# Performance work log

Hardware: AMD Instinct MI355X
Metric: run time of the kernel (lower is better)

The kernel has to match this reference:

```python
import jax, jax.numpy as jnp
import numpy as np

WS = 8
NUM_HEADS = 4
DIM = 64
H = W = 128
B = 16
EPS = 1e-5


def _rel_pos_index(ws):
    coords = np.stack(np.meshgrid(np.arange(ws), np.arange(ws), indexing='ij'))  # (2,ws,ws)
    cf = coords.reshape(2, -1)
    rel = (cf[:, :, None] - cf[:, None, :]).transpose(1, 2, 0).astype(np.int64)
    rel[..., 0] += ws - 1
    rel[..., 1] += ws - 1
    rel[..., 0] *= 2 * ws - 1
    return jnp.asarray(rel.sum(-1))  # (ws*ws, ws*ws)

_RPI = _rel_pos_index(WS)


def _ln_hw(x, g, b):
    # LayerNorm over last two dims (H,W) of (B,C,H,W), affine shape (H,W)
    mu = x.mean(axis=(-2, -1), keepdims=True)
    var = ((x - mu) ** 2).mean(axis=(-2, -1), keepdims=True)
    return (x - mu) / jnp.sqrt(var + EPS) * g + b


def _ln_c(x, g, b):
    mu = x.mean(-1, keepdims=True)
    var = ((x - mu) ** 2).mean(-1, keepdims=True)
    return (x - mu) / jnp.sqrt(var + EPS) * g + b


def _win_part(x, ws):
    # (B,C,H,W) -> (B*nW, ws*ws, C)
    b, c, hh, ww = x.shape
    x = x.reshape(b, c, hh // ws, ws, ww // ws, ws)
    return x.transpose(0, 2, 4, 3, 5, 1).reshape(b * (hh // ws) * (ww // ws), ws * ws, c)


def _win_rev(w, ws, hh, ww, b):
    # (B*nW, ws*ws, C) -> (B,C,H,W)
    c = w.shape[-1]
    w = w.reshape(b, hh // ws, ww // ws, ws, ws, c)
    return w.transpose(0, 5, 1, 3, 2, 4).reshape(b, c, hh, ww)


def _forward(x, lclg1_ln1_g, lclg1_ln1_b, lclg1_conv_w, lclg1_conv_b, lclg1_ln2_g, lclg1_ln2_b,
             lclg2_ln1_g, lclg2_ln1_b, lclg2_conv_w, lclg2_conv_b, lclg2_ln2_g, lclg2_ln2_b,
             pos1, pos2, q_w, q_b, kv_w, kv_b, rpb_table, gamma, proj_w, proj_b,
             norm2_g, norm2_b, fc1_w, fc1_b, fc2_w, fc2_b):
    b, c, hh, ww = x.shape
    h = NUM_HEADS
    hd = c // h
    n = WS * WS
    scale = hd ** -0.5

    def lclg(z, g1, b1, cw, cb, g2, b2):
        z = _ln_hw(z, g1, b1)
        z = jnp.einsum('oc,bchw->bohw', cw, z) + cb[None, :, None, None]  # 1x1 conv
        return jax.nn.gelu(_ln_hw(z, g2, b2), approximate=False)

    x1 = lclg(x, lclg1_ln1_g, lclg1_ln1_b, lclg1_conv_w, lclg1_conv_b, lclg1_ln2_g, lclg1_ln2_b)
    x2 = lclg(x, lclg2_ln1_g, lclg2_ln1_b, lclg2_conv_w, lclg2_conv_b, lclg2_ln2_g, lclg2_ln2_b)

    x1w = _win_part(x1, WS) + pos1  # (B_, N, C)
    x2w = _win_part(x2, WS) + pos2
    bw = x1w.shape[0]

    q = (x1w @ q_w.T + q_b).reshape(bw, n, h, hd).transpose(0, 2, 1, 3) * scale  # (B_,h,N,hd)
    kv = (x2w @ kv_w.T + kv_b).reshape(bw, n, 2, h, hd).transpose(2, 0, 3, 1, 4)
    k, v = kv[0], kv[1]

    attn = jnp.einsum('bhnd,bhmd->bhnm', q, k)
    bias = rpb_table[_RPI.reshape(-1)].reshape(n, n, h).transpose(2, 0, 1)  # (h,N,N)
    attn = jax.nn.softmax(attn + bias[None], axis=-1)
    o = jnp.einsum('bhnm,bhmd->bhnd', attn, v)  # (B_,h,N,hd)

    # LAM_Module: attention over head_dim channels of (B_,h,N,hd)
    y = o.transpose(0, 3, 1, 2).reshape(bw, hd, h * n)  # (B_,hd,h*N)
    energy = jnp.einsum('bik,bjk->bij', y, y)  # (B_,hd,hd)
    lam = jnp.einsum('bij,bjk->bik', jax.nn.softmax(energy, axis=-1), y)
    y = (gamma * lam + y).reshape(bw, hd, h, n).transpose(0, 2, 3, 1)  # (B_,h,N,hd)

    xo = y.transpose(0, 2, 1, 3).reshape(bw, n, c) + q.transpose(0, 2, 1, 3).reshape(bw, n, c) + x1w
    xo = xo @ proj_w.T + proj_b

    xo = _win_rev(xo, WS, hh, ww, b)  # (B,C,H,W)

    # MLP with pre-norm residual over channel dim
    t = xo.reshape(b, c, hh * ww).transpose(0, 2, 1)  # (B,HW,C)
    tn = _ln_c(t, norm2_g, norm2_b)
    t = t + (jax.nn.gelu(tn @ fc1_w.T + fc1_b, approximate=False) @ fc2_w.T + fc2_b)
    return t.transpose(0, 2, 1).reshape(b, c, hh, ww)


def setup_inputs() -> dict:
    key = jax.random.key(0)
    ks = jax.random.split(key, 16)
    d = DIM

    def rn(i, shape, sc=0.02):
        return jax.random.normal(ks[i], shape, jnp.float32) * sc

    return dict(
        x=jax.random.normal(ks[0], (B, d, H, W), jnp.float32),
        lclg1_ln1_g=jnp.ones((H, W), jnp.float32), lclg1_ln1_b=jnp.zeros((H, W), jnp.float32),
        lclg1_conv_w=rn(1, (d, d)), lclg1_conv_b=jnp.zeros((d,), jnp.float32),
        lclg1_ln2_g=jnp.ones((H, W), jnp.float32), lclg1_ln2_b=jnp.zeros((H, W), jnp.float32),
        lclg2_ln1_g=jnp.ones((H, W), jnp.float32), lclg2_ln1_b=jnp.zeros((H, W), jnp.float32),
        lclg2_conv_w=rn(2, (d, d)), lclg2_conv_b=jnp.zeros((d,), jnp.float32),
        lclg2_ln2_g=jnp.ones((H, W), jnp.float32), lclg2_ln2_b=jnp.zeros((H, W), jnp.float32),
        pos1=jnp.ones((1, WS * WS, d), jnp.float32),
        pos2=jnp.ones((1, WS * WS, d), jnp.float32),
        q_w=rn(3, (d, d)), q_b=jnp.zeros((d,), jnp.float32),
        kv_w=rn(4, (2 * d, d)), kv_b=jnp.zeros((2 * d,), jnp.float32),
        rpb_table=rn(5, ((2 * WS - 1) ** 2, NUM_HEADS)),
        gamma=jnp.full((1,), 0.1, jnp.float32),
        proj_w=rn(6, (d, d)), proj_b=jnp.zeros((d,), jnp.float32),
        norm2_g=jnp.ones((d,), jnp.float32), norm2_b=jnp.zeros((d,), jnp.float32),
        fc1_w=rn(7, (d, d)), fc1_b=jnp.zeros((d,), jnp.float32),
        fc2_w=rn(8, (d, d)), fc2_b=jnp.zeros((d,), jnp.float32),
    )


def reference(x, lclg1_ln1_g, lclg1_ln1_b, lclg1_conv_w, lclg1_conv_b, lclg1_ln2_g, lclg1_ln2_b,
              lclg2_ln1_g, lclg2_ln1_b, lclg2_conv_w, lclg2_conv_b, lclg2_ln2_g, lclg2_ln2_b,
              pos1, pos2, q_w, q_b, kv_w, kv_b, rpb_table, gamma, proj_w, proj_b,
              norm2_g, norm2_b, fc1_w, fc1_b, fc2_w, fc2_b):
    return _forward(x, lclg1_ln1_g, lclg1_ln1_b, lclg1_conv_w, lclg1_conv_b, lclg1_ln2_g, lclg1_ln2_b,
                    lclg2_ln1_g, lclg2_ln1_b, lclg2_conv_w, lclg2_conv_b, lclg2_ln2_g, lclg2_ln2_b,
                    pos1, pos2, q_w, q_b, kv_w, kv_b, rpb_table, gamma, proj_w, proj_b,
                    norm2_g, norm2_b, fc1_w, fc1_b, fc2_w, fc2_b)
```

## Files before the change

### kernel.cpp

```cpp
#include <hip/hip_runtime.h>
#include <hip/hip_bf16.h>

typedef __hip_bfloat16 bf16;
typedef __attribute__((ext_vector_type(8))) short short8;
typedef __attribute__((ext_vector_type(4))) short short4v;
typedef __attribute__((ext_vector_type(4))) float float4v;
typedef __attribute__((ext_vector_type(2))) float float2v;

__device__ __forceinline__ short f2bs(float f){
    union { bf16 h; short s; } u; u.h = __float2bfloat16(f); return u.s;
}
__device__ __forceinline__ float bs2f(short s){
    return __uint_as_float(((unsigned)(unsigned short)s) << 16);
}
__device__ __forceinline__ float gelu_exact(float x){
    float ax = fabsf(x) * 0.70710678118654752440f;
    float t  = __builtin_amdgcn_rcpf(fmaf(0.3275911f, ax, 1.0f));
    float poly = t*fmaf(t, fmaf(t, fmaf(t, fmaf(t, 1.061405429f, -1.453152027f),
                                 1.421413741f), -0.284496736f), 0.254829592f);
    float e = __expf(-ax*ax);
    float erfp = fmaf(-poly, e, 1.0f);
    float er = copysignf(erfp, x);
    return 0.5f * x * (1.0f + er);
}
#define MFMA(a,b,c) __builtin_amdgcn_mfma_f32_16x16x32_bf16((a),(b),(c),0,0,0)

#define HW 16384
#define NPLANE 1048576
#define EPS 1e-5f
#define LS 72

#define OFF_W1   0
#define OFF_W2   4096
#define OFF_QW   8192
#define OFF_KVW  12288
#define OFF_PW   20480
#define OFF_FW1  24576
#define OFF_FW2  28672

__global__ __launch_bounds__(256) void k_pre(const float* __restrict__ x,
                                             float* __restrict__ mu,
                                             float* __restrict__ rinv,
                                             const float* __restrict__ w1, const float* __restrict__ w2,
                                             const float* __restrict__ qw, const float* __restrict__ kvw,
                                             const float* __restrict__ pw, const float* __restrict__ fw1,
                                             const float* __restrict__ fw2,
                                             short* __restrict__ wb, float* __restrict__ rowsum){
    int bi = blockIdx.x;
    int tid = threadIdx.x;
    if (bi < 1024){
        const float* p = x + (size_t)bi * HW;
        float s = 0.f, ss = 0.f;
        for (int i = tid; i < HW/4; i += 256){
            float4v v = *(const float4v*)(p + i*4);
            #pragma unroll
            for (int k = 0; k < 4; k++){ s += v[k]; ss += v[k]*v[k]; }
        }
        __shared__ float rs[256], rss[256];
        rs[tid] = s; rss[tid] = ss; __syncthreads();
        for (int st = 128; st > 0; st >>= 1){
            if (tid < st){ rs[tid] += rs[tid+st]; rss[tid] += rss[tid+st]; }
            __syncthreads();
        }
        if (tid == 0){
            float m = rs[0] * (1.f/HW);
            float v = rss[0] * (1.f/HW) - m*m;
            mu[bi] = m; rinv[bi] = rsqrtf(v + EPS);
        }
    } else if (bi < 1032){
        int wi = bi - 1024;
        const float* src = wi==0?w1: wi==1?w2: wi==2?qw: wi==3?kvw: wi==4?(kvw+4096): wi==5?pw: wi==6?fw1: fw2;
        short* dst = wb + wi*4096;
        int base = tid*16;
        short8 o8[2];
        #pragma unroll
        for (int k = 0; k < 2; k++){
            float4v v0 = *(const float4v*)(src + base + 8*k);
            float4v v1 = *(const float4v*)(src + base + 8*k + 4);
            #pragma unroll
            for (int j = 0; j < 4; j++){ o8[k][j] = f2bs(v0[j]); o8[k][4+j] = f2bs(v1[j]); }
        }
        *(short8*)&dst[base]     = o8[0];
        *(short8*)&dst[base + 8] = o8[1];
    } else {
        if (tid < 128){
            int br = tid >> 6, o = tid & 63;
            const float* W = br ? w2 : w1;
            float s = 0.f;
            for (int c = 0; c < 64; c++) s += W[o*64 + c];
            rowsum[br*64 + o] = s;
        }
    }
}

__global__ __launch_bounds__(256, 4) void k_conv(const float* __restrict__ x,
                                              const float* __restrict__ mu,
                                              const float* __restrict__ rinv,
                                              const float* __restrict__ g1a, const float* __restrict__ b1a,
                                              const float* __restrict__ cb1,
                                              const float* __restrict__ g1b, const float* __restrict__ b1b,
                                              const float* __restrict__ cb2,
                                              const short* __restrict__ wb,
                                              const float* __restrict__ rowsum,
                                              float* __restrict__ partS, float* __restrict__ partQ){
    int blk = blockIdx.x;
    int b = blk >> 6; int chunk = blk & 63;
    __shared__ __align__(16) short xn_bf[64*LS];
    const int tid = threadIdx.x;
    const int wq = tid >> 6, lane = tid & 63, qd = lane >> 4, col = lane & 15;
    const float4v zf = {0.f,0.f,0.f,0.f};
    const int p = tid & 63, cq = tid >> 6;

    float4v m4[4], r4[4];
    #pragma unroll
    for (int k = 0; k < 4; k++){
        m4[k] = *(const float4v*)(mu   + b*64 + 16*cq + 4*k);
        r4[k] = *(const float4v*)(rinv + b*64 + 16*cq + 4*k);
    }
    short8 a10 = *(const short8*)&wb[OFF_W1 + (16*wq + col)*64 + 8*qd];
    short8 a11 = *(const short8*)&wb[OFF_W1 + (16*wq + col)*64 + 32 + 8*qd];
    short8 a20 = *(const short8*)&wb[OFF_W2 + (16*wq + col)*64 + 8*qd];
    short8 a21 = *(const short8*)&wb[OFF_W2 + (16*wq + col)*64 + 32 + 8*qd];
    float cb1v[4], rs1v[4], cb2v[4], rs2v[4];
    #pragma unroll
    for (int r = 0; r < 4; r++){
        int o = 16*wq + 4*qd + r;
        cb1v[r] = cb1[o]; rs1v[r] = rowsum[o];
        cb2v[r] = cb2[o]; rs2v[r] = rowsum[64 + o];
    }
    float sa[2][4]  = {{0.f,0.f,0.f,0.f},{0.f,0.f,0.f,0.f}};
    float ssa[2][4] = {{0.f,0.f,0.f,0.f},{0.f,0.f,0.f,0.f}};

    for (int tl = 0; tl < 4; tl++){
        int hw0 = chunk*256 + tl*64;
        {
            const float* xb = x + (size_t)(b*64 + 16*cq)*HW + hw0 + p;
            short8 o8[2];
            #pragma unroll
            for (int k = 0; k < 2; k++)
                #pragma unroll
                for (int j = 0; j < 8; j++){
                    int jj = 8*k + j;
                    float v = xb[(size_t)jj*HW];
                    o8[k][j] = f2bs((v - m4[jj>>2][jj&3]) * r4[jj>>2][jj&3]);
                }
            *(short8*)&xn_bf[p*LS + 16*cq]     = o8[0];
            *(short8*)&xn_bf[p*LS + 16*cq + 8] = o8[1];
        }
        __syncthreads();
        #pragma unroll
        for (int jn = 0; jn < 4; jn++){
            short8 bx0 = *(const short8*)&xn_bf[(16*jn + col)*LS + 8*qd];
            short8 bx1 = *(const short8*)&xn_bf[(16*jn + col)*LS + 32 + 8*qd];
            int hw = hw0 + 16*jn + col;
            {
                float4v acc = zf;
                acc = MFMA(a10, bx0, acc);
                acc = MFMA(a11, bx1, acc);
                float gl = g1a[hw], bl = b1a[hw];
                #pragma unroll
                for (int r = 0; r < 4; r++){
                    float v = gl*acc[r] + bl*rs1v[r] + cb1v[r];
                    sa[0][r] += v; ssa[0][r] += v*v;
                }
            }
            {
                float4v acc = zf;
                acc = MFMA(a20, bx0, acc);
                acc = MFMA(a21, bx1, acc);
                float gl = g1b[hw], bl = b1b[hw];
                #pragma unroll
                for (int r = 0; r < 4; r++){
                    float v = gl*acc[r] + bl*rs2v[r] + cb2v[r];
                    sa[1][r] += v; ssa[1][r] += v*v;
                }
            }
        }
        __syncthreads();
    }

    #pragma unroll
    for (int br = 0; br < 2; br++)
        #pragma unroll
        for (int r = 0; r < 4; r++){
            float s = sa[br][r], ss = ssa[br][r];
            s += __shfl_xor(s, 1); ss += __shfl_xor(ss, 1);
            s += __shfl_xor(s, 2); ss += __shfl_xor(ss, 2);
            s += __shfl_xor(s, 4); ss += __shfl_xor(ss, 4);
            s += __shfl_xor(s, 8); ss += __shfl_xor(ss, 8);
            if (col == 0){
                int o = 16*wq + 4*qd + r;
                size_t pi = ((size_t)(br*16 + b)*64 + o)*64 + chunk;
                partS[pi] = s; partQ[pi] = ss;
            }
        }
}

__global__ __launch_bounds__(256) void k_fin(const float* __restrict__ partS,
                                             const float* __restrict__ partQ,
                                             float* __restrict__ mu2,
                                             float* __restrict__ rinv2){
    int row = blockIdx.x*4 + (threadIdx.x >> 6);
    int lane = threadIdx.x & 63;
    float s  = partS[(size_t)row*64 + lane];
    float ss = partQ[(size_t)row*64 + lane];
    #pragma unroll
    for (int st = 1; st < 64; st <<= 1){
        s  += __shfl_xor(s,  st);
        ss += __shfl_xor(ss, st);
    }
    if (lane == 0){
        float m = s * (1.f/HW);
        float v = ss * (1.f/HW) - m*m;
        mu2[row] = m; rinv2[row] = rsqrtf(v + EPS);
    }
}

__global__ __launch_bounds__(256, 4) void k_attn(const float* __restrict__ x, float* __restrict__ outp,
                                              const float* __restrict__ mu1, const float* __restrict__ rinv1,
                                              const float* __restrict__ rowsum,
                                              const float* __restrict__ cb1, const float* __restrict__ cb2,
                                              const float* __restrict__ g1a, const float* __restrict__ b1a,
                                              const float* __restrict__ g1b, const float* __restrict__ b1b,
                                              const float* __restrict__ mu2, const float* __restrict__ rinv2,
                                              const float* __restrict__ g2a, const float* __restrict__ b2a,
                                              const float* __restrict__ g2b, const float* __restrict__ b2b,
                                              const float* __restrict__ pos1, const float* __restrict__ pos2,
                                              const short* __restrict__ wb,
                                              const float* __restrict__ qb, const float* __restrict__ kvb,
                                              const float* __restrict__ rpb, const float* __restrict__ gammap,
                                              const float* __restrict__ pb,
                                              const float* __restrict__ n2g, const float* __restrict__ n2b,
                                              const float* __restrict__ fb1,
                                              const float* __restrict__ fb2){
    int B = blockIdx.x;
    int hy = (B & 7) | ((B >> 5) & 8);
    int wx = (((B >> 9) & 7) << 1) | ((B >> 3) & 1);
    int b  = (B >> 4) & 15;

    const short* qwb  = wb + OFF_QW;
    const short* kvwb = wb + OFF_KVW;
    const short* pwb  = wb + OFF_PW;
    const short* f1b  = wb + OFF_FW1;
    const short* f2b  = wb + OFF_FW2;

    __shared__ __align__(16) char smem[40464];
    short* bufA = (short*)smem;
    short* bufK = (short*)(smem + 9216);
    short* bufV = (short*)(smem + 18432);
    short* bufQ = (short*)(smem + 27648);
    float* rpb_lds = (float*)(smem + 36864);
    float* energyS = (float*)(smem + 36864);
    short* soft_bf = (short*)(smem + 37888);
    float* XOf  = (float*)(smem + 18432);
    short* tnb  = (short*)smem;
    short* h1b  = (short*)(smem + 9216);
    float* sumS = (float*)(smem + 36864);
    float* sqS  = (float*)(smem + 37888);
    float* muS  = (float*)(smem + 38912);
    float* rinvS= (float*)(smem + 39168);

    const int tid = threadIdx.x;
    const int wq = tid >> 6, lane = tid & 63, qd = lane >> 4, col = lane & 15;
    size_t base = (size_t)b * NPLANE;
    #define HWOF(t) ((hy*8 + ((t)>>3))*128 + wx*8 + ((t)&7))

    const float4v zf = {0.f,0.f,0.f,0.f};
    const short8 zero8 = {0,0,0,0,0,0,0,0};

    for (int i = tid; i < 900; i += 256) rpb_lds[i] = rpb[i];

    {
        int t = tid & 63, cq = tid >> 6;
        int hw = HWOF(t);
        const float* mup = mu1   + b*64 + 16*cq;
        const float* rvp = rinv1 + b*64 + 16*cq;
        float4v m4[4], r4[4];
        #pragma unroll
        for (int k = 0; k < 4; k++){
            m4[k] = *(const float4v*)(mup + 4*k);
            r4[k] = *(const float4v*)(rvp + 4*k);
        }
        short8 o8[2];
        #pragma unroll
        for (int k = 0; k < 2; k++)
            #pragma unroll
            for (int j = 0; j < 8; j++){
                int jj = 8*k + j;
                float v = x[base + (size_t)(16*cq + jj)*HW + hw];
                o8[k][j] = f2bs((v - m4[jj>>2][jj&3]) * r4[jj>>2][jj&3]);
            }
        *(short8*)&bufV[t*LS + 16*cq]     = o8[0];
        *(short8*)&bufV[t*LS + 16*cq + 8] = o8[1];
    }
    __syncthreads();

    {
        short8 a10 = *(const short8*)&wb[OFF_W1 + (16*wq + col)*64 + 8*qd];
        short8 a11 = *(const short8*)&wb[OFF_W1 + (16*wq + col)*64 + 32 + 8*qd];
        short8 a20 = *(const short8*)&wb[OFF_W2 + (16*wq + col)*64 + 8*qd];
        short8 a21 = *(const short8*)&wb[OFF_W2 + (16*wq + col)*64 + 32 + 8*qd];
        float cb1v[4], rs1v[4], m2a[4], rv2a[4];
        float cb2v[4], rs2v[4], m2b[4], rv2b[4];
        #pragma unroll
        for (int r = 0; r < 4; r++){
            int o = 16*wq + 4*qd + r;
            cb1v[r] = cb1[o]; rs1v[r] = rowsum[o];
            m2a[r] = mu2[b*64 + o]; rv2a[r] = rinv2[b*64 + o];
            cb2v[r] = cb2[o]; rs2v[r] = rowsum[64 + o];
            m2b[r] = mu2[1024 + b*64 + o]; rv2b[r] = rinv2[1024 + b*64 + o];
        }
        #pragma unroll
        for (int jn = 0; jn < 4; jn++){
            int t = 16*jn + col; int hw = HWOF(t);
            short8 bx0 = *(const short8*)&bufV[t*LS + 8*qd];
            short8 bx1 = *(const short8*)&bufV[t*LS + 32 + 8*qd];
            {
                float4v acc = zf;
                acc = MFMA(a10, bx0, acc);
                acc = MFMA(a11, bx1, acc);
                float gl = g1a[hw], bl = b1a[hw], gg = g2a[hw], bo = b2a[hw];
                float4v p4 = *(const float4v*)(pos1 + t*64 + 16*wq + 4*qd);
                short4v pk;
                #pragma unroll
                for (int r = 0; r < 4; r++){
                    float v = gl*acc[r] + bl*rs1v[r] + cb1v[r];
                    float z = (v - m2a[r]) * rv2a[r] * gg + bo;
                    pk[r] = f2bs(gelu_exact(z) + p4[r]);
                }
                *(short4v*)&bufA[t*LS + 16*wq + 4*qd] = pk;
            }
            {
                float4v acc = zf;
                acc = MFMA(a20, bx0, acc);
                acc = MFMA(a21, bx1, acc);
                float gl = g1b[hw], bl = b1b[hw], gg = g2b[hw], bo = b2b[hw];
                float4v p4 = *(const float4v*)(pos2 + t*64 + 16*wq + 4*qd);
                short4v pk;
                #pragma unroll
                for (int r = 0; r < 4; r++){
                    float v = gl*acc[r] + bl*rs2v[r] + cb2v[r];
                    float z = (v - m2b[r]) * rv2b[r] * gg + bo;
                    pk[r] = f2bs(gelu_exact(z) + p4[r]);
                }
                *(short4v*)&bufQ[t*LS + 16*wq + 4*qd] = pk;
            }
        }
    }
    __syncthreads();

    {
        short8 ax0 = *(const short8*)&bufQ[(16*wq + col)*LS + 8*qd];
        short8 ax1 = *(const short8*)&bufQ[(16*wq + col)*LS + 32 + 8*qd];
        #pragma unroll
        for (int jn = 0; jn < 4; jn++){
            int c = 16*jn + col;
            short8 wv0 = *(const short8*)&kvwb[(64 + c)*64 + 8*qd];
            short8 wv1 = *(const short8*)&kvwb[(64 + c)*64 + 32 + 8*qd];
            float4v acc = zf;
            acc = MFMA(ax0, wv0, acc);
            acc = MFMA(ax1, wv1, acc);
            float bv = kvb[64 + c];
            short4v pk;
            #pragma unroll
            for (int r = 0; r < 4; r++) pk[r] = f2bs(acc[r] + bv);
            *(short4v*)&bufV[c*LS + 16*wq + 4*qd] = pk;
        }
        short8 a0 = *(const short8*)&kvwb[(16*wq + col)*64 + 8*qd];
        short8 a1 = *(const short8*)&kvwb[(16*wq + col)*64 + 32 + 8*qd];
        float kbr[4];
        #pragma unroll
        for (int r = 0; r < 4; r++) kbr[r] = kvb[16*wq + 4*qd + r];
        #pragma unroll
        for (int jn = 0; jn < 4; jn++){
            int t = 16*jn + col;
            short8 bx0 = *(const short8*)&bufQ[t*LS + 8*qd];
            short8 bx1 = *(const short8*)&bufQ[t*LS + 32 + 8*qd];
            float4v acc = zf;
            acc = MFMA(a0, bx0, acc);
            acc = MFMA(a1, bx1, acc);
            short4v pk;
            #pragma unroll
            for (int r = 0; r < 4; r++) pk[r] = f2bs(acc[r] + kbr[r]);
            *(short4v*)&bufK[t*LS + 16*wq + 4*qd] = pk;
        }
    }
    __syncthreads();

    {
        short8 a0 = *(const short8*)&qwb[(16*wq + col)*64 + 8*qd];
        short8 a1 = *(const short8*)&qwb[(16*wq + col)*64 + 32 + 8*qd];
        float qbr[4];
        #pragma unroll
        for (int r = 0; r < 4; r++) qbr[r] = qb[16*wq + 4*qd + r];
        #pragma unroll
        for (int jn = 0; jn < 4; jn++){
            int t = 16*jn + col;
            short8 bx0 = *(const short8*)&bufA[t*LS + 8*qd];
            short8 bx1 = *(const short8*)&bufA[t*LS + 32 + 8*qd];
            float4v acc = zf;
            acc = MFMA(a0, bx0, acc);
            acc = MFMA(a1, bx1, acc);
            short4v pk;
            #pragma unroll
            for (int r = 0; r < 4; r++) pk[r] = f2bs((acc[r] + qbr[r]) * 0.25f);
            *(short4v*)&bufQ[t*LS + 16*wq + 4*qd] = pk;
        }
    }
    short4v xreg[4];
    #pragma unroll
    for (int h = 0; h < 4; h++){
        short4v xr;
        #pragma unroll
        for (int r = 0; r < 4; r++)
            xr[r] = bufA[(16*wq + 4*qd + r)*LS + 16*h + col];
        xreg[h] = xr;
    }
    __syncthreads();

    int idx_t[4][4];
    {
        int t = 16*wq + col, ty = t >> 3, tx = t & 7;
        #pragma unroll
        for (int jn = 0; jn < 4; jn++)
            #pragma unroll
            for (int r = 0; r < 4; r++){
                int u = 16*jn + 4*qd + r;
                idx_t[jn][r] = (ty - (u>>3) + 7)*15 + (tx - (u&7) + 7);
            }
    }

    for (int h = 0; h < 4; h++){
        short8 bq = *(const short8*)&bufQ[(16*wq + col)*LS + h*16 + (qd & 1)*8];
        float pr[4][4];
        #pragma unroll
        for (int jn = 0; jn < 4; jn++){
            short8 ak = *(const short8*)&bufK[(16*jn + col)*LS + h*16 + (qd & 1)*8];
            if (qd >= 2) ak = zero8;
            float4v acc = MFMA(ak, bq, zf);
            #pragma unroll
            for (int r = 0; r < 4; r++)
                pr[jn][r] = acc[r] + rpb_lds[idx_t[jn][r]*4 + h];
        }
        float m = pr[0][0];
        #pragma unroll
        for (int jn = 0; jn < 4; jn++)
            #pragma unroll
            for (int r = 0; r < 4; r++) m = fmaxf(m, pr[jn][r]);
        m = fmaxf(m, __shfl_xor(m, 16));
        m = fmaxf(m, __shfl_xor(m, 32));
        float s = 0.f;
        #pragma unroll
        for (int jn = 0; jn < 4; jn++)
            #pragma unroll
            for (int r = 0; r < 4; r++){ pr[jn][r] = __expf(pr[jn][r] - m); s += pr[jn][r]; }
        s += __shfl_xor(s, 16);
        s += __shfl_xor(s, 32);
        float rc = 1.f / s;
        #pragma unroll
        for (int jn = 0; jn < 4; jn++){
            short4v pk;
            #pragma unroll
            for (int r = 0; r < 4; r++) pk[r] = f2bs(pr[jn][r] * rc);
            *(short4v*)&bufA[(16*wq + col)*LS + 16*jn + 4*qd] = pk;
        }
        short8 ap0 = *(const short8*)&bufA[(16*wq + col)*LS + 8*qd];
        short8 ap1 = *(const short8*)&bufA[(16*wq + col)*LS + 32 + 8*qd];
        short8 bv0 = *(const short8*)&bufV[(h*16 + col)*LS + 8*qd];
        short8 bv1 = *(const short8*)&bufV[(h*16 + col)*LS + 32 + 8*qd];
        float4v acc_o = zf;
        acc_o = MFMA(ap0, bv0, acc_o);
        acc_o = MFMA(ap1, bv1, acc_o);
        __syncthreads();
        short4v ot;
        #pragma unroll
        for (int r = 0; r < 4; r++) ot[r] = f2bs(acc_o[r]);
        *(short4v*)&bufV[(h*16 + col)*LS + 16*wq + 4*qd] = ot;
        #pragma unroll
        for (int r = 0; r < 4; r++)
            bufK[(16*wq + 4*qd + r)*LS + h*16 + col] = ot[r];
    }
    __syncthreads();

    {
        float4v acc_e = zf;
        #pragma unroll
        for (int h = 0; h < 4; h++){
            short8 f0 = *(const short8*)&bufV[(h*16 + col)*LS + 8*qd];
            short8 f1 = *(const short8*)&bufV[(h*16 + col)*LS + 32 + 8*qd];
            acc_e = MFMA(f0, f0, acc_e);
            acc_e = MFMA(f1, f1, acc_e);
        }
        if (wq == 0){
            #pragma unroll
            for (int r = 0; r < 4; r++) energyS[(4*qd + r)*16 + col] = acc_e[r];
        }
    }
    __syncthreads();
    if (tid < 16){
        int i = tid; float m = -1e30f;
        for (int j = 0; j < 16; j++) m = fmaxf(m, energyS[i*16 + j]);
        float s = 0.f; float e[16];
        for (int j = 0; j < 16; j++){ e[j] = __expf(energyS[i*16 + j] - m); s += e[j]; }
        float rc = 1.f / s;
        for (int j = 0; j < 16; j++) soft_bf[i*32 + j] = f2bs(e[j] * rc);
        for (int j = 0; j < 16; j++) soft_bf[i*32 + 16 + j] = 0;
    }
    __syncthreads();

    {
        float gam = gammap[0];
        short8 asf = *(const short8*)&soft_bf[col*32 + 8*qd];
        #pragma unroll
        for (int h = 0; h < 4; h++){
            short8 ay = *(const short8*)&bufK[(16*wq + col)*LS + 16*h + (qd & 1)*8];
            float4v acc = MFMA(ay, asf, zf);
            short4v xv = xreg[h];
            #pragma unroll
            for (int r = 0; r < 4; r++){
                int ro = (16*wq + 4*qd + r)*LS + 16*h + col;
                float ot = bs2f(bufK[ro]);
                float qv = bs2f(bufQ[ro]);
                float xo = gam*acc[r] + ot + qv + bs2f(xv[r]);
                bufK[ro] = f2bs(xo);
            }
        }
    }
    __syncthreads();

    {
        short8 a0 = *(const short8*)&pwb[(16*wq + col)*64 + 8*qd];
        short8 a1 = *(const short8*)&pwb[(16*wq + col)*64 + 32 + 8*qd];
        float pbr[4];
        #pragma unroll
        for (int r = 0; r < 4; r++) pbr[r] = pb[16*wq + 4*qd + r];
        #pragma unroll
        for (int jn = 0; jn < 4; jn++){
            int t = 16*jn + col;
            short8 bx0 = *(const short8*)&bufK[t*LS + 8*qd];
            short8 bx1 = *(const short8*)&bufK[t*LS + 32 + 8*qd];
            float4v acc = zf;
            acc = MFMA(a0, bx0, acc);
            acc = MFMA(a1, bx1, acc);
            float2v w0 = {acc[0]+pbr[0], acc[1]+pbr[1]};
            float2v w1 = {acc[2]+pbr[2], acc[3]+pbr[3]};
            *(float2v*)&XOf[t*66 + 16*wq + 4*qd]     = w0;
            *(float2v*)&XOf[t*66 + 16*wq + 4*qd + 2] = w1;
        }
    }
    __syncthreads();

    {
        int p = tid & 63, qg = tid >> 6;
        float s = 0.f, ss = 0.f;
        #pragma unroll
        for (int j = 0; j < 8; j++){
            float2v v = *(const float2v*)&XOf[p*66 + qg*16 + 2*j];
            s += v[0]+v[1]; ss += v[0]*v[0] + v[1]*v[1];
        }
        sumS[qg*64 + p] = s; sqS[qg*64 + p] = ss;
    }
    __syncthreads();
    if (tid < 64){
        float s  = sumS[tid] + sumS[64+tid] + sumS[128+tid] + sumS[192+tid];
        float ss = sqS[tid]  + sqS[64+tid]  + sqS[128+tid]  + sqS[192+tid];
        float m = s * (1.f/64.f);
        float var = ss * (1.f/64.f) - m*m;
        muS[tid] = m; rinvS[tid] = rsqrtf(var + EPS);
    }
    __syncthreads();
    {
        int p = tid & 63, qg = tid >> 6;
        float m = muS[p], rv = rinvS[p];
        short8 o8[2];
        #pragma unroll
        for (int k = 0; k < 2; k++)
            #pragma unroll
            for (int j = 0; j < 8; j++){
                int c = qg*16 + k*8 + j;
                o8[k][j] = f2bs((XOf[p*66 + c] - m) * rv * n2g[c] + n2b[c]);
            }
        *(short8*)&tnb[p*LS + qg*16]     = o8[0];
        *(short8*)&tnb[p*LS + qg*16 + 8] = o8[1];
    }
    __syncthreads();
    {
        short8 a0 = *(const short8*)&f1b[(16*wq + col)*64 + 8*qd];
        short8 a1 = *(const short8*)&f1b[(16*wq + col)*64 + 32 + 8*qd];
        float fbr[4];
        #pragma unroll
        for (int r = 0; r < 4; r++) fbr[r] = fb1[16*wq + 4*qd + r];
        #pragma unroll
        for (int jn = 0; jn < 4; jn++){
            int t = 16*jn + col;
            short8 bx0 = *(const short8*)&tnb[t*LS + 8*qd];
            short8 bx1 = *(const short8*)&tnb[t*LS + 32 + 8*qd];
            float4v acc = zf;
            acc = MFMA(a0, bx0, acc);
            acc = MFMA(a1, bx1, acc);
            short4v pk;
            #pragma unroll
            for (int r = 0; r < 4; r++) pk[r] = f2bs(gelu_exact(acc[r] + fbr[r]));
            *(short4v*)&h1b[t*LS + 16*wq + 4*qd] = pk;
        }
    }
    __syncthreads();
    {
        short8 a0 = *(const short8*)&h1b[(16*wq + col)*LS + 8*qd];
        short8 a1 = *(const short8*)&h1b[(16*wq + col)*LS + 32 + 8*qd];
        #pragma unroll
        for (int jn = 0; jn < 4; jn++){
            int c2 = 16*jn + col;
            short8 f0 = *(const short8*)&f2b[c2*64 + 8*qd];
            short8 f1 = *(const short8*)&f2b[c2*64 + 32 + 8*qd];
            float4v acc = zf;
            acc = MFMA(a0, f0, acc);
            acc = MFMA(a1, f1, acc);
            float bv = fb2[c2];
            float4v ov;
            #pragma unroll
            for (int r = 0; r < 4; r++)
                ov[r] = acc[r] + bv + XOf[(16*wq + 4*qd + r)*66 + c2];
            int t0 = 16*wq + 4*qd;
            *(float4v*)(outp + base + (size_t)c2*HW + HWOF(t0)) = ov;
        }
    }
    #undef HWOF
}

extern "C" void kernel_launch(void* const* d_in, const int* in_sizes, int n_in,
                              void* d_out, int out_size, void* d_ws, size_t ws_size,
                              hipStream_t stream){
    const float* x        = (const float*)d_in[0];
    const float* l1_g1    = (const float*)d_in[1];
    const float* l1_b1    = (const float*)d_in[2];
    const float* l1_cw    = (const float*)d_in[3];
    const float* l1_cb    = (const float*)d_in[4];
    const float* l1_g2    = (const float*)d_in[5];
    const float* l1_b2    = (const float*)d_in[6];
    const float* l2_g1    = (const float*)d_in[7];
    const float* l2_b1    = (const float*)d_in[8];
    const float* l2_cw    = (const float*)d_in[9];
    const float* l2_cb    = (const float*)d_in[10];
    const float* l2_g2    = (const float*)d_in[11];
    const float* l2_b2    = (const float*)d_in[12];
    const float* pos1     = (const float*)d_in[13];
    const float* pos2     = (const float*)d_in[14];
    const float* q_w      = (const float*)d_in[15];
    const float* q_b      = (const float*)d_in[16];
    const float* kv_w     = (const float*)d_in[17];
    const float* kv_b     = (const float*)d_in[18];
    const float* rpb      = (const float*)d_in[19];
    const float* gamma    = (const float*)d_in[20];
    const float* proj_w   = (const float*)d_in[21];
    const float* proj_b   = (const float*)d_in[22];
    const float* norm2_g  = (const float*)d_in[23];
    const float* norm2_b  = (const float*)d_in[24];
    const float* fc1_w    = (const float*)d_in[25];
    const float* fc1_b    = (const float*)d_in[26];
    const float* fc2_w    = (const float*)d_in[27];
    const float* fc2_b    = (const float*)d_in[28];

    float* out = (float*)d_out;

    float* partS = (float*)d_ws;
    float* partQ = partS + (size_t)2048*64;
    float* mu1   = partQ + (size_t)2048*64;
    float* rinv1 = mu1 + 1024;
    float* mu2   = rinv1 + 1024;
    float* rinv2 = mu2 + 2048;
    float* rowsumG = rinv2 + 2048;
    short* wbuf  = (short*)(rowsumG + 128);

    k_pre  <<<1033, 256, 0, stream>>>(x, mu1, rinv1,
                                      l1_cw, l2_cw, q_w, kv_w, proj_w, fc1_w, fc2_w,
                                      wbuf, rowsumG);
    k_conv <<<1024, 256, 0, stream>>>(x, mu1, rinv1,
                                      l1_g1, l1_b1, l1_cb,
                                      l2_g1, l2_b1, l2_cb,
                                      wbuf, rowsumG,
                                      partS, partQ);
    k_fin  <<<512, 256, 0, stream>>>(partS, partQ, mu2, rinv2);
    k_attn <<<4096, 256, 0, stream>>>(x, out, mu1, rinv1, rowsumG,
                                      l1_cb, l2_cb,
                                      l1_g1, l1_b1, l2_g1, l2_b1,
                                      mu2, rinv2,
                                      l1_g2, l1_b2, l2_g2, l2_b2,
                                      pos1, pos2, wbuf, q_b, kv_b,
                                      rpb, gamma, proj_b,
                                      norm2_g, norm2_b, fc1_b, fc2_b);
}
```

Baseline: 316.5 us.

## Cache normalized bf16 input in window layout from conv pass for attention kernel

```diff
diff --git a/kernel.cpp b/kernel.cpp
--- a/kernel.cpp
+++ b/kernel.cpp
@@ -14,14 +14,7 @@
     return __uint_as_float(((unsigned)(unsigned short)s) << 16);
 }
 __device__ __forceinline__ float gelu_exact(float x){
-    float ax = fabsf(x) * 0.70710678118654752440f;
-    float t  = __builtin_amdgcn_rcpf(fmaf(0.3275911f, ax, 1.0f));
-    float poly = t*fmaf(t, fmaf(t, fmaf(t, fmaf(t, 1.061405429f, -1.453152027f),
-                                 1.421413741f), -0.284496736f), 0.254829592f);
-    float e = __expf(-ax*ax);
-    float erfp = fmaf(-poly, e, 1.0f);
-    float er = copysignf(erfp, x);
-    return 0.5f * x * (1.0f + er);
+    return 0.5f * x * (1.0f + erff(x * 0.70710678118654752440f));
 }
 #define MFMA(a,b,c) __builtin_amdgcn_mfma_f32_16x16x32_bf16((a),(b),(c),0,0,0)
 
@@ -102,6 +95,7 @@
                                               const float* __restrict__ cb2,
                                               const short* __restrict__ wb,
                                               const float* __restrict__ rowsum,
+                                              short* __restrict__ xw,
                                               float* __restrict__ partS, float* __restrict__ partQ){
     int blk = blockIdx.x;
     int b = blk >> 6; int chunk = blk & 63;
@@ -146,6 +140,13 @@
                 }
             *(short8*)&xn_bf[p*LS + 16*cq]     = o8[0];
             *(short8*)&xn_bf[p*LS + 16*cq + 8] = o8[1];
+            int hw = hw0 + p;
+            int row = hw >> 7, cc = hw & 127;
+            int win = (row >> 3)*16 + (cc >> 3);
+            int t   = (row & 7)*8 + (cc & 7);
+            short* dst = xw + ((((size_t)(b*256 + win)) << 6) + t)*64 + 16*cq;
+            *(short8*)&dst[0] = o8[0];
+            *(short8*)&dst[8] = o8[1];
         }
         __syncthreads();
         #pragma unroll
@@ -216,8 +217,7 @@
     }
 }
 
-__global__ __launch_bounds__(256, 4) void k_attn(const float* __restrict__ x, float* __restrict__ outp,
-                                              const float* __restrict__ mu1, const float* __restrict__ rinv1,
+__global__ __launch_bounds__(256, 4) void k_attn(const short* __restrict__ xw, float* __restrict__ outp,
                                               const float* __restrict__ rowsum,
                                               const float* __restrict__ cb1, const float* __restrict__ cb2,
                                               const float* __restrict__ g1a, const float* __restrict__ b1a,
@@ -237,6 +237,7 @@
     int hy = (B & 7) | ((B >> 5) & 8);
     int wx = (((B >> 9) & 7) << 1) | ((B >> 3) & 1);
     int b  = (B >> 4) & 15;
+    int win = hy*16 + wx;
 
     const short* qwb  = wb + OFF_QW;
     const short* kvwb = wb + OFF_KVW;
@@ -271,27 +272,12 @@
     for (int i = tid; i < 900; i += 256) rpb_lds[i] = rpb[i];
 
     {
-        int t = tid & 63, cq = tid >> 6;
-        int hw = HWOF(t);
-        const float* mup = mu1   + b*64 + 16*cq;
-        const float* rvp = rinv1 + b*64 + 16*cq;
-        float4v m4[4], r4[4];
-        #pragma unroll
-        for (int k = 0; k < 4; k++){
-            m4[k] = *(const float4v*)(mup + 4*k);
-            r4[k] = *(const float4v*)(rvp + 4*k);
-        }
-        short8 o8[2];
-        #pragma unroll
-        for (int k = 0; k < 2; k++)
-            #pragma unroll
-            for (int j = 0; j < 8; j++){
-                int jj = 8*k + j;
-                float v = x[base + (size_t)(16*cq + jj)*HW + hw];
-                o8[k][j] = f2bs((v - m4[jj>>2][jj&3]) * r4[jj>>2][jj&3]);
-            }
-        *(short8*)&bufV[t*LS + 16*cq]     = o8[0];
-        *(short8*)&bufV[t*LS + 16*cq + 8] = o8[1];
+        int t = tid >> 2, c0 = (tid & 3) << 4;
+        const short* src = xw + (((size_t)(b*256 + win)) << 12) + t*64 + c0;
+        short8 v0 = *(const short8*)src;
+        short8 v1 = *(const short8*)(src + 8);
+        *(short8*)&bufV[t*LS + c0]     = v0;
+        *(short8*)&bufV[t*LS + c0 + 8] = v1;
     }
     __syncthreads();
 
@@ -663,7 +649,8 @@
 
     float* out = (float*)d_out;
 
-    float* partS = (float*)d_ws;
+    short* xw    = (short*)d_ws;
+    float* partS = (float*)(xw + (size_t)16*256*4096);
     float* partQ = partS + (size_t)2048*64;
     float* mu1   = partQ + (size_t)2048*64;
     float* rinv1 = mu1 + 1024;
@@ -678,10 +665,10 @@
     k_conv <<<1024, 256, 0, stream>>>(x, mu1, rinv1,
                                       l1_g1, l1_b1, l1_cb,
                                       l2_g1, l2_b1, l2_cb,
-                                      wbuf, rowsumG,
+                                      wbuf, rowsumG, xw,
                                       partS, partQ);
     k_fin  <<<512, 256, 0, stream>>>(partS, partQ, mu2, rinv2);
-    k_attn <<<4096, 256, 0, stream>>>(x, out, mu1, rinv1, rowsumG,
+    k_attn <<<4096, 256, 0, stream>>>(xw, out, rowsumG,
                                       l1_cb, l2_cb,
                                       l1_g1, l1_b1, l2_g1, l2_b1,
                                       mu2, rinv2,
```

After: 334.0 us. 1.06x slower.
